# Performance work log

Hardware: AMD Instinct MI355X
Metric: run time of the kernel (lower is better)

The kernel has to match this reference:

```python
import jax, jax.numpy as jnp
import numpy as np

N = 524288
B, F, H, W = 2, 4, 64, 512
S = B * F * H * W  # dense voxel segment space
EPS = 1e-5


def _bn(x, g, b):
    # BatchNorm1d in training mode: normalize over the point dim with biased var
    m = x.mean(0)
    v = jnp.mean((x - m) ** 2, 0)
    return (x - m) / jnp.sqrt(v + EPS) * g + b


def setup_inputs() -> dict:
    key = jax.random.key(0)
    ks = jax.random.split(key, 20)
    pts = jax.random.normal(ks[0], (N, 4), dtype=jnp.float32) * 10.0
    bcol = jax.random.randint(ks[1], (N, 1), 0, B)
    fcol = jax.random.randint(ks[2], (N, 1), 0, F)
    hcol = jax.random.randint(ks[3], (N, 1), 0, H)
    wcol = jax.random.randint(ks[4], (N, 1), 0, W)
    coors = jnp.concatenate([bcol, fcol, hcol, wcol], -1).astype(jnp.int32)
    # original reads batch_size/frame_size from coors[-1]
    coors = coors.at[-1].set(jnp.array([B - 1, F - 1, H - 1, W - 1], dtype=jnp.int32))
    s = 0.02
    p = {
        'pre_gamma': jnp.ones((8,), jnp.float32),
        'pre_beta': jnp.zeros((8,), jnp.float32),
        'W1': jax.random.normal(ks[5], (8, 64), jnp.float32) * s,
        'g1': jnp.ones((64,), jnp.float32), 'b1': jnp.zeros((64,), jnp.float32),
        'W2': jax.random.normal(ks[6], (64, 128), jnp.float32) * s,
        'g2': jnp.ones((128,), jnp.float32), 'b2': jnp.zeros((128,), jnp.float32),
        'W3': jax.random.normal(ks[7], (128, 256), jnp.float32) * s,
        'g3': jnp.ones((256,), jnp.float32), 'b3': jnp.zeros((256,), jnp.float32),
        'W4': jax.random.normal(ks[8], (256, 256), jnp.float32) * s,
        'b4': jnp.zeros((256,), jnp.float32),
        'Wc': jax.random.normal(ks[9], (256, 64), jnp.float32) * s,
        'bc': jnp.zeros((64,), jnp.float32),
    }
    return {'pts': pts, 'pts_coors': coors, **p}


def reference(pts, pts_coors, pre_gamma, pre_beta, W1, g1, b1, W2, g2, b2,
              W3, g3, b3, W4, b4, Wc, bc):
    c = pts_coors
    lin = ((c[:, 0] * F + c[:, 1]) * H + c[:, 2]) * W + c[:, 3]  # (N,)
    counts = jax.ops.segment_sum(jnp.ones((pts.shape[0],), pts.dtype), lin, num_segments=S)
    # with_distance
    dist = jnp.linalg.norm(pts[:, :3], axis=1, keepdims=True)
    # with_cluster_center: scatter_mean then gather
    vsum = jax.ops.segment_sum(pts, lin, num_segments=S)
    vmean = vsum / jnp.clip(counts, 1.0)[:, None]
    f_cluster = pts[:, :3] - vmean[lin][:, :3]
    feats = jnp.concatenate([pts, dist, f_cluster], -1)  # (N, 8)
    feats = _bn(feats, pre_gamma, pre_beta)  # pre_norm
    x = jax.nn.relu(_bn(feats @ W1, g1, b1))
    x = jax.nn.relu(_bn(x @ W2, g2, b2))
    x = jax.nn.relu(_bn(x @ W3, g3, b3))
    point_feats = x @ W4 + b4  # (N, 256)
    # scatter_max over voxels
    seg = jax.ops.segment_max(point_feats, lin, num_segments=S)
    mask = (counts > 0)[:, None]
    voxel_feats = jnp.where(mask, seg, 0.0)
    comp = jax.nn.relu(voxel_feats @ Wc + bc)
    comp = jnp.where(mask, comp, 0.0)  # empty voxels stay zero in stack_frame
    stack = comp.reshape(B, F, H, W, -1)  # (B, F, H, W, Cc)
    residual = jnp.concatenate([stack[:, -1] - stack[:, f] for f in range(F - 1)], -1)
    residual_img = jnp.transpose(residual, (0, 3, 1, 2))  # (B, C, H, W)
    return residual_img
```

## Files before the change

kernel.cpp:

```cpp
#include <hip/hip_runtime.h>
#include <hip/hip_bf16.h>
#include <stdint.h>

typedef unsigned int u32;
typedef unsigned short u16;
typedef __attribute__((ext_vector_type(8))) short bf16x8;
typedef __attribute__((ext_vector_type(4))) float f32x4;

#define NPTS 524288
#define FF 4
#define HH 64
#define WW 512
#define SS 262144
#define EPSV 1e-5f
#define NB 8192
#define RCAP 80
#define VCAP 80

__device__ __forceinline__ float bf2f(u16 h){ return __uint_as_float(((u32)h)<<16); }
__device__ __forceinline__ u16 f2bf(float f){
  u32 u = __float_as_uint(f);
  return (u16)((u + 0x7FFFu + ((u>>16)&1u)) >> 16);
}

__device__ __forceinline__ void point_feats(int p, const float* __restrict__ pts,
    const u32* __restrict__ lin, const u32* __restrict__ counts,
    const float* __restrict__ vsum, float f[8], u32* vout){
  float4 pt = ((const float4*)pts)[p];
  u32 v = lin[p];
  float cnt = fmaxf((float)counts[v], 1.0f);
  float inv = 1.0f/cnt;
  float mx = vsum[v*3+0]*inv, my = vsum[v*3+1]*inv, mz = vsum[v*3+2]*inv;
  float dist = sqrtf(pt.x*pt.x + pt.y*pt.y + pt.z*pt.z);
  f[0]=pt.x; f[1]=pt.y; f[2]=pt.z; f[3]=pt.w; f[4]=dist;
  f[5]=pt.x-mx; f[6]=pt.y-my; f[7]=pt.z-mz;
  *vout = v;
}

__global__ __launch_bounds__(256) void k_lin(const float* __restrict__ pts,
                                             const int* __restrict__ coors,
                                             u32* __restrict__ lin,
                                             u32* __restrict__ counts,
                                             float* __restrict__ vsum){
  int p = blockIdx.x*256 + threadIdx.x;
  int4 c = ((const int4*)coors)[p];
  u32 v = ((u32)((c.x*FF + c.y)*HH + c.z))*WW + (u32)c.w;
  lin[p] = v;
  atomicAdd(&counts[v], 1u);
  float4 pt = ((const float4*)pts)[p];
  atomicAdd(&vsum[v*3+0], pt.x);
  atomicAdd(&vsum[v*3+1], pt.y);
  atomicAdd(&vsum[v*3+2], pt.z);
}

__global__ __launch_bounds__(256) void k_scan_a(const u32* __restrict__ counts,
                                                u32* __restrict__ blockSums){
  __shared__ u32 lds[256];
  int b = blockIdx.x, t = threadIdx.x;
  uint4 c4 = ((const uint4*)counts)[b*256 + t];
  lds[t] = c4.x + c4.y + c4.z + c4.w;
  __syncthreads();
  for(int s=128; s>0; s>>=1){ if(t<s) lds[t] += lds[t+s]; __syncthreads(); }
  if(t==0) blockSums[b] = lds[0];
}

__global__ void k_scan_b(u32* blockSums){
  if(threadIdx.x==0){
    u32 run = 0;
    for(int i=0;i<256;i++){ u32 v = blockSums[i]; blockSums[i] = run; run += v; }
  }
}

__global__ __launch_bounds__(256) void k_scan_c(const u32* __restrict__ counts,
                                                const u32* __restrict__ blockSums,
                                                u32* __restrict__ offsets,
                                                u32* __restrict__ cursor){
  __shared__ u32 lds[256];
  int b = blockIdx.x, t = threadIdx.x;
  uint4 c4 = ((const uint4*)counts)[b*256 + t];
  u32 mysum = c4.x + c4.y + c4.z + c4.w;
  lds[t] = mysum;
  __syncthreads();
  for(int d=1; d<256; d<<=1){
    u32 v = (t>=d) ? lds[t-d] : 0u;
    __syncthreads();
    lds[t] += v;
    __syncthreads();
  }
  u32 off = blockSums[b] + (t>0 ? lds[t-1] : 0u);
  u32 base = (u32)(b*1024 + t*4);
  offsets[base+0]=off; cursor[base+0]=off; off += c4.x;
  offsets[base+1]=off; cursor[base+1]=off; off += c4.y;
  offsets[base+2]=off; cursor[base+2]=off; off += c4.z;
  offsets[base+3]=off; cursor[base+3]=off; off += c4.w;
  if(base+4 == SS) offsets[SS] = off;
}

__global__ __launch_bounds__(256) void k_scatter(const u32* __restrict__ lin,
                                                 u32* __restrict__ cursor,
                                                 u32* __restrict__ order){
  int p = blockIdx.x*256 + threadIdx.x;
  u32 v = lin[p];
  u32 pos = atomicAdd(&cursor[v], 1u);
  order[pos] = p;
}

__global__ __launch_bounds__(256) void k_prep(const float* __restrict__ W2,
    const float* __restrict__ W3, const float* __restrict__ W4,
    const float* __restrict__ Wc,
    u16* __restrict__ W2t, u16* __restrict__ W3t, u16* __restrict__ W4t,
    u16* __restrict__ Wct){
  int i = blockIdx.x*256 + threadIdx.x;
  if(i < 8192){
    int k = i >> 7, n = i & 127;
    W2t[n*64 + k] = f2bf(W2[i]);
  } else if(i < 8192+32768){
    int j = i - 8192;
    int k = j >> 8, n = j & 255;
    W3t[n*128 + k] = f2bf(W3[j]);
  } else if(i < 8192+32768+65536){
    int j = i - (8192+32768);
    int k = j >> 8, n = j & 255;
    W4t[n*256 + k] = f2bf(W4[j]);
  } else if(i < 8192+32768+65536+16384){
    int j = i - (8192+32768+65536);
    int k = j >> 6, n = j & 63;
    Wct[n*256 + k] = f2bf(Wc[j]);
  }
}

__global__ __launch_bounds__(256) void k_stats0(const float* __restrict__ pts,
    const u32* __restrict__ lin, const u32* __restrict__ counts,
    const float* __restrict__ vsum, float* __restrict__ sum0, float* __restrict__ sq0){
  int p = blockIdx.x*256 + threadIdx.x;
  float f[8]; u32 v;
  point_feats(p, pts, lin, counts, vsum, f, &v);
  __shared__ float lsum[4][8], lsq[4][8];
  int lane = threadIdx.x & 63, wv = threadIdx.x >> 6;
  #pragma unroll
  for(int c=0;c<8;c++){
    float s = f[c], q = f[c]*f[c];
    #pragma unroll
    for(int d=32; d; d>>=1){ s += __shfl_xor(s,d); q += __shfl_xor(q,d); }
    if(lane==0){ lsum[wv][c]=s; lsq[wv][c]=q; }
  }
  __syncthreads();
  if(threadIdx.x<8){
    float s=0.f,q=0.f;
    for(int g=0;g<4;g++){ s+=lsum[g][threadIdx.x]; q+=lsq[g][threadIdx.x]; }
    atomicAdd(&sum0[threadIdx.x], s);
    atomicAdd(&sq0[threadIdx.x], q);
  }
}

__global__ void k_fold(const float* __restrict__ sum, const float* __restrict__ sq,
                       const float* __restrict__ g, const float* __restrict__ b,
                       float* __restrict__ a, float* __restrict__ c, int C){
  int i = blockIdx.x*64 + threadIdx.x;
  if(i < C){
    float m = sum[i]*(1.0f/NPTS);
    float v = sq[i]*(1.0f/NPTS) - m*m;
    v = fmaxf(v, 0.0f);
    float ai = g[i] / sqrtf(v + EPSV);
    a[i] = ai;
    c[i] = b[i] - m*ai;
  }
}

__global__ __launch_bounds__(256) void k_stats1(const float* __restrict__ pts,
    const u32* __restrict__ lin, const u32* __restrict__ counts,
    const float* __restrict__ vsum,
    const float* __restrict__ a0, const float* __restrict__ c0,
    const float* __restrict__ W1, float* __restrict__ sum1, float* __restrict__ sq1){
  __shared__ float ws[4][64], wq[4][64];
  int t = threadIdx.x;
  int p = blockIdx.x*256 + t;
  float f[8]; u32 v;
  point_feats(p, pts, lin, counts, vsum, f, &v);
  float y0[8];
  #pragma unroll
  for(int k=0;k<8;k++) y0[k] = a0[k]*f[k] + c0[k];
  float z[64];
  #pragma unroll
  for(int j=0;j<64;j++){
    float s=0.f;
    #pragma unroll
    for(int k=0;k<8;k++) s += y0[k]*W1[k*64+j];
    z[j]=s;
  }
  int lane = t&63, wv = t>>6;
  float ks=0.f, kq=0.f;
  #pragma unroll
  for(int c=0;c<64;c++){
    float s=z[c], q=z[c]*z[c];
    #pragma unroll
    for(int d=1; d<64; d<<=1){ s+=__shfl_xor(s,d); q+=__shfl_xor(q,d); }
    if(lane==c){ ks=s; kq=q; }
  }
  ws[wv][lane]=ks; wq[wv][lane]=kq;
  __syncthreads();
  if(t<64){
    float S=ws[0][t]+ws[1][t]+ws[2][t]+ws[3][t];
    float Q=wq[0][t]+wq[1][t]+wq[2][t]+wq[3][t];
    atomicAdd(&sum1[t],S); atomicAdd(&sq1[t],Q);
  }
}

__global__ __launch_bounds__(256,2) void k_mstats2(
    const float* __restrict__ pts, const u32* __restrict__ lin,
    const u32* __restrict__ counts, const float* __restrict__ vsum,
    const float* __restrict__ a0, const float* __restrict__ c0,
    const float* __restrict__ a1, const float* __restrict__ c1,
    const float* __restrict__ W1, const u16* __restrict__ W2t,
    float* __restrict__ sum2, float* __restrict__ sq2){
  __shared__ u16 T1[256*72];
  int tid = threadIdx.x, lane = tid&63, wid = tid>>6, l15 = lane&15, lg = lane>>4;
  float s2[2] = {0.f,0.f}, q2[2] = {0.f,0.f};

  for(int cch=0; cch<4; cch++){
    int p = blockIdx.x*1024 + cch*256 + tid;
    float f[8]; u32 v;
    point_feats(p, pts, lin, counts, vsum, f, &v);
    float y0[8];
    #pragma unroll
    for(int k=0;k<8;k++) y0[k] = a0[k]*f[k] + c0[k];
    u32 pk[32];
    #pragma unroll
    for(int jj=0;jj<32;jj++){
      float s0=0.f, s1=0.f;
      #pragma unroll
      for(int k=0;k<8;k++){ s0 += y0[k]*W1[k*64+2*jj]; s1 += y0[k]*W1[k*64+2*jj+1]; }
      float v0f = fmaxf(a1[2*jj]*s0   + c1[2*jj],   0.f);
      float v1f = fmaxf(a1[2*jj+1]*s1 + c1[2*jj+1], 0.f);
      pk[jj] = (u32)f2bf(v0f) | ((u32)f2bf(v1f)<<16);
    }
    __syncthreads();
    {
      uint4* dst = (uint4*)&T1[tid*72];
      #pragma unroll
      for(int q=0;q<8;q++) dst[q] = make_uint4(pk[4*q],pk[4*q+1],pk[4*q+2],pk[4*q+3]);
    }
    __syncthreads();
    #pragma unroll
    for(int ci=0; ci<2; ci++){
      int ch = (wid + 4*ci)*16 + l15;
      const u16* wb = W2t + (size_t)ch*64 + lg*8;
      bf16x8 b0 = *(const bf16x8*)(wb);
      bf16x8 b1 = *(const bf16x8*)(wb + 32);
      for(int rt=0; rt<16; rt++){
        const u16* ap = T1 + (rt*16 + l15)*72 + lg*8;
        bf16x8 af0 = *(const bf16x8*)(ap);
        bf16x8 af1 = *(const bf16x8*)(ap + 32);
        f32x4 acc = {0.f,0.f,0.f,0.f};
        acc = __builtin_amdgcn_mfma_f32_16x16x32_bf16(af0, b0, acc, 0,0,0);
        acc = __builtin_amdgcn_mfma_f32_16x16x32_bf16(af1, b1, acc, 0,0,0);
        #pragma unroll
        for(int i=0;i<4;i++){ s2[ci] += acc[i]; q2[ci] += acc[i]*acc[i]; }
      }
    }
  }
  #pragma unroll
  for(int ci=0; ci<2; ci++){
    float s = s2[ci], q = q2[ci];
    s += __shfl_xor(s,16); s += __shfl_xor(s,32);
    q += __shfl_xor(q,16); q += __shfl_xor(q,32);
    if(lg == 0){
      int ch = (wid + 4*ci)*16 + l15;
      atomicAdd(&sum2[ch], s);
      atomicAdd(&sq2[ch], q);
    }
  }
}

__global__ __launch_bounds__(256,1) void k_chain2(
    const float* __restrict__ pts, const u32* __restrict__ lin,
    const u32* __restrict__ counts, const float* __restrict__ vsum,
    const u32* __restrict__ order,
    const float* __restrict__ a0, const float* __restrict__ c0,
    const float* __restrict__ a1, const float* __restrict__ c1,
    const float* __restrict__ a2, const float* __restrict__ c2,
    const float* __restrict__ W1, const u16* __restrict__ W2t,
    const u16* __restrict__ W3t,
    u32* __restrict__ y2s,
    float* __restrict__ sum3, float* __restrict__ sq3){
  __shared__ u16 T1[256*72];
  __shared__ u16 T2[256*136];
  int tid = threadIdx.x, lane = tid&63, wid = tid>>6, l15 = lane&15, lg = lane>>4;
  float s3[4] = {0.f,0.f,0.f,0.f}, q3[4] = {0.f,0.f,0.f,0.f};

  for(int cch=0; cch<4; cch++){
    int rr = blockIdx.x*1024 + cch*256 + tid;
    int p = (int)order[rr];
    float f[8]; u32 v;
    point_feats(p, pts, lin, counts, vsum, f, &v);
    float y0[8];
    #pragma unroll
    for(int k=0;k<8;k++) y0[k] = a0[k]*f[k] + c0[k];
    u32 pk[32];
    #pragma unroll
    for(int jj=0;jj<32;jj++){
      float s0=0.f, s1=0.f;
      #pragma unroll
      for(int k=0;k<8;k++){ s0 += y0[k]*W1[k*64+2*jj]; s1 += y0[k]*W1[k*64+2*jj+1]; }
      float v0f = fmaxf(a1[2*jj]*s0   + c1[2*jj],   0.f);
      float v1f = fmaxf(a1[2*jj+1]*s1 + c1[2*jj+1], 0.f);
      pk[jj] = (u32)f2bf(v0f) | ((u32)f2bf(v1f)<<16);
    }
    __syncthreads();
    {
      uint4* dst = (uint4*)&T1[tid*72];
      #pragma unroll
      for(int q=0;q<8;q++) dst[q] = make_uint4(pk[4*q],pk[4*q+1],pk[4*q+2],pk[4*q+3]);
    }
    __syncthreads();
    #pragma unroll
    for(int ci=0; ci<2; ci++){
      int ch = (wid + 4*ci)*16 + l15;
      const u16* wb = W2t + (size_t)ch*64 + lg*8;
      bf16x8 b0 = *(const bf16x8*)(wb);
      bf16x8 b1 = *(const bf16x8*)(wb + 32);
      float a2v = a2[ch], c2v = c2[ch];
      for(int rt=0; rt<16; rt++){
        const u16* ap = T1 + (rt*16 + l15)*72 + lg*8;
        bf16x8 af0 = *(const bf16x8*)(ap);
        bf16x8 af1 = *(const bf16x8*)(ap + 32);
        f32x4 acc = {0.f,0.f,0.f,0.f};
        acc = __builtin_amdgcn_mfma_f32_16x16x32_bf16(af0, b0, acc, 0,0,0);
        acc = __builtin_amdgcn_mfma_f32_16x16x32_bf16(af1, b1, acc, 0,0,0);
        int rbase = rt*16 + lg*4;
        #pragma unroll
        for(int i=0;i<4;i++)
          T2[(rbase+i)*136 + ch] = f2bf(fmaxf(a2v*acc[i] + c2v, 0.f));
      }
    }
    __syncthreads();
    {
      const u32* T2w = (const u32*)T2;
      u32 base = (u32)blockIdx.x*1024u + (u32)cch*256u;
      for(int i=tid; i<256*64; i+=256){
        int row = i>>6, w = i&63;
        y2s[(size_t)(base+row)*64 + w] = T2w[row*68 + w];
      }
    }
    #pragma unroll
    for(int ci=0; ci<4; ci++){
      int ch = (wid + 4*ci)*16 + l15;
      const u16* wb = W3t + (size_t)ch*128 + lg*8;
      bf16x8 b[4];
      #pragma unroll
      for(int ks=0; ks<4; ks++) b[ks] = *(const bf16x8*)(wb + ks*32);
      for(int rt=0; rt<16; rt++){
        const u16* ap = T2 + (rt*16 + l15)*136 + lg*8;
        f32x4 acc = {0.f,0.f,0.f,0.f};
        #pragma unroll
        for(int ks=0; ks<4; ks++){
          bf16x8 af = *(const bf16x8*)(ap + ks*32);
          acc = __builtin_amdgcn_mfma_f32_16x16x32_bf16(af, b[ks], acc, 0,0,0);
        }
        #pragma unroll
        for(int i=0;i<4;i++){ s3[ci] += acc[i]; q3[ci] += acc[i]*acc[i]; }
      }
    }
  }
  #pragma unroll
  for(int ci=0; ci<4; ci++){
    float s = s3[ci], q = q3[ci];
    s += __shfl_xor(s,16); s += __shfl_xor(s,32);
    q += __shfl_xor(q,16); q += __shfl_xor(q,32);
    if(lg == 0){
      int ch = (wid + 4*ci)*16 + l15;
      atomicAdd(&sum3[ch], s);
      atomicAdd(&sq3[ch], q);
    }
  }
}

__global__ __launch_bounds__(512,4) void k_mega6(
    const u32* __restrict__ offsets, const u32* __restrict__ y2s,
    const float* __restrict__ a3, const float* __restrict__ c3,
    const u16* __restrict__ W3t, const u16* __restrict__ W4t,
    const u16* __restrict__ Wct,
    const float* __restrict__ b4, const float* __restrict__ bc,
    u16* __restrict__ comp){
  __shared__ __align__(16) char SM[78208];
  u16* T3  = (u16*)(SM);
  u16* T2s = (u16*)(SM + 42240);
  u16* Tz0 = (u16*)(SM + 42240);
  u16* Tz1 = (u16*)(SM + 53760);
  u16* TA  = (u16*)(SM + 65280);
  u32* vst = (u32*)(SM + 76800);
  float* bb = (float*)(SM + 77152);
  u32* hdr = (u32*)(SM + 78176);

  int tid = threadIdx.x, lane = tid & 63, wid = tid >> 6;
  int l15 = lane & 15, lg = lane >> 4;
  int cg = wid & 3, rh = wid >> 2;
  int nvt = rh ? 2 : 3, vt0 = rh ? 3 : 0;

  if(tid == 0){
    u32 t0 = (u32)blockIdx.x * 64u;
    u32 lo=0, hi=SS;
    while(lo<hi){ u32 mid=(lo+hi)>>1; if(offsets[mid] < t0) lo=mid+1; else hi=mid; }
    u32 vlo = lo, vhi;
    if(blockIdx.x == NB-1) vhi = SS;
    else {
      u32 t1 = t0 + 64u;
      lo = vlo; hi = SS;
      while(lo<hi){ u32 mid=(lo+hi)>>1; if(offsets[mid] < t1) lo=mid+1; else hi=mid; }
      vhi = lo;
    }
    hdr[0]=vlo; hdr[1]=vhi; hdr[2]=offsets[vlo]; hdr[3]=offsets[vhi];
  }
  if(tid < 256) bb[tid] = b4[tid];
  __syncthreads();
  u32 vlo=hdr[0], vhi=hdr[1], start=hdr[2], end=hdr[3];
  int R = (int)(end - start); if(R > RCAP) R = RCAP;
  int V = (int)(vhi - vlo);   if(V > VCAP) V = VCAP;

  if(tid <= VCAP){
    u32 o = (tid <= V) ? offsets[vlo + tid] : end;
    int s = (int)(o - start); if(s > RCAP) s = RCAP;
    vst[tid] = (u32)s;
  }

  {
    u32* T2w = (u32*)T2s;
    for(int i=tid; i<RCAP*64; i+=512){
      int row = i>>6, w = i&63;
      u32 val = (row < R) ? y2s[(size_t)(start+row)*64 + w] : 0u;
      T2w[row*68 + w] = val;
    }
  }
  __syncthreads();

  for(int ci=0; ci<2; ci++){
    int ch = (wid + 8*ci)*16 + l15;
    const u16* wb = W3t + (size_t)ch*128 + lg*8;
    bf16x8 b[4];
    #pragma unroll
    for(int ks=0; ks<4; ks++) b[ks] = *(const bf16x8*)(wb + ks*32);
    float a3v = a3[ch], c3v = c3[ch];
    for(int rt=0; rt<5; rt++){
      const u16* ap = T2s + (rt*16 + l15)*136 + lg*8;
      f32x4 acc = {0.f,0.f,0.f,0.f};
      #pragma unroll
      for(int ks=0; ks<4; ks++){
        bf16x8 af = *(const bf16x8*)(ap + ks*32);
        acc = __builtin_amdgcn_mfma_f32_16x16x32_bf16(af, b[ks], acc, 0,0,0);
      }
      int rbase = rt*16 + lg*4;
      #pragma unroll
      for(int i=0;i<4;i++)
        T3[(rbase+i)*264 + ch] = f2bf(fmaxf(a3v*acc[i] + c3v, 0.f));
    }
  }
  __syncthreads();

  f32x4 acc3[3];
  #pragma unroll
  for(int i=0;i<3;i++) acc3[i] = (f32x4){0.f,0.f,0.f,0.f};
  int ch4 = cg*16 + l15;

  for(int pr=0; pr<2; pr++){
    int oc0 = 2*pr, oc1 = 2*pr + 1;
    {
      const u16* wb0 = W4t + (size_t)(oc0*64 + ch4)*256 + lg*8;
      const u16* wb1 = W4t + (size_t)(oc1*64 + ch4)*256 + lg*8;
      bf16x8 b0[8], b1[8];
      #pragma unroll
      for(int ks=0; ks<8; ks++){
        b0[ks] = *(const bf16x8*)(wb0 + ks*32);
        b1[ks] = *(const bf16x8*)(wb1 + ks*32);
      }
      int rtB = rh ? 3 : 0, rtE = rh ? 5 : 3;
      for(int rt=rtB; rt<rtE; rt++){
        const u16* ap = T3 + (rt*16 + l15)*264 + lg*8;
        f32x4 aA = {0.f,0.f,0.f,0.f}, aB = {0.f,0.f,0.f,0.f};
        #pragma unroll
        for(int ks=0; ks<8; ks++){
          bf16x8 af = *(const bf16x8*)(ap + ks*32);
          aA = __builtin_amdgcn_mfma_f32_16x16x32_bf16(af, b0[ks], aA, 0,0,0);
          aB = __builtin_amdgcn_mfma_f32_16x16x32_bf16(af, b1[ks], aB, 0,0,0);
        }
        int rbase = rt*16 + lg*4;
        #pragma unroll
        for(int i=0;i<4;i++){
          Tz0[(rbase+i)*72 + ch4] = f2bf(aA[i]);
          Tz1[(rbase+i)*72 + ch4] = f2bf(aB[i]);
        }
      }
    }
    __syncthreads();
    for(int i=tid; i<VCAP*64; i+=512){
      int v = i>>6, k = i&63;
      u32 r0 = vst[v], r1 = vst[v+1];
      u16 outv = 0;
      if(r1 > r0){
        float m = -3.0e38f;
        for(u32 r=r0; r<r1; r++) m = fmaxf(m, bf2f(Tz0[r*72+k]));
        outv = f2bf(m + bb[oc0*64+k]);
      }
      TA[v*72+k] = outv;
    }
    __syncthreads();
    {
      const u16* wb = Wct + (size_t)ch4*256 + oc0*64 + lg*8;
      bf16x8 c0f = *(const bf16x8*)(wb);
      bf16x8 c1f = *(const bf16x8*)(wb + 32);
      #pragma unroll
      for(int s=0; s<3; s++){
        if(s < nvt){
          int vt = vt0 + s;
          const u16* ap = TA + (vt*16 + l15)*72 + lg*8;
          bf16x8 af0 = *(const bf16x8*)(ap);
          bf16x8 af1 = *(const bf16x8*)(ap + 32);
          acc3[s] = __builtin_amdgcn_mfma_f32_16x16x32_bf16(af0, c0f, acc3[s], 0,0,0);
          acc3[s] = __builtin_amdgcn_mfma_f32_16x16x32_bf16(af1, c1f, acc3[s], 0,0,0);
        }
      }
    }
    __syncthreads();
    for(int i=tid; i<VCAP*64; i+=512){
      int v = i>>6, k = i&63;
      u32 r0 = vst[v], r1 = vst[v+1];
      u16 outv = 0;
      if(r1 > r0){
        float m = -3.0e38f;
        for(u32 r=r0; r<r1; r++) m = fmaxf(m, bf2f(Tz1[r*72+k]));
        outv = f2bf(m + bb[oc1*64+k]);
      }
      TA[v*72+k] = outv;
    }
    __syncthreads();
    {
      const u16* wb = Wct + (size_t)ch4*256 + oc1*64 + lg*8;
      bf16x8 c0f = *(const bf16x8*)(wb);
      bf16x8 c1f = *(const bf16x8*)(wb + 32);
      #pragma unroll
      for(int s=0; s<3; s++){
        if(s < nvt){
          int vt = vt0 + s;
          const u16* ap = TA + (vt*16 + l15)*72 + lg*8;
          bf16x8 af0 = *(const bf16x8*)(ap);
          bf16x8 af1 = *(const bf16x8*)(ap + 32);
          acc3[s] = __builtin_amdgcn_mfma_f32_16x16x32_bf16(af0, c0f, acc3[s], 0,0,0);
          acc3[s] = __builtin_amdgcn_mfma_f32_16x16x32_bf16(af1, c1f, acc3[s], 0,0,0);
        }
      }
    }
    __syncthreads();
  }

  {
    float bcv = bc[ch4];
    #pragma unroll
    for(int s=0; s<3; s++){
      if(s < nvt){
        int vt = vt0 + s;
        int vbase = vt*16 + lg*4;
        #pragma unroll
        for(int i=0;i<4;i++){
          int vox = vbase + i;
          if(vox < V){
            bool nz = vst[vox+1] > vst[vox];
            float val = nz ? fmaxf(acc3[s][i] + bcv, 0.f) : 0.f;
            comp[(size_t)(vlo+vox)*64 + ch4] = f2bf(val);
          }
        }
      }
    }
  }
}

__global__ __launch_bounds__(256) void k_resid(const u16* __restrict__ comp,
                                               float* __restrict__ out){
  __shared__ u32 cl[4*128*32];
  int t = threadIdx.x;
  int blk = blockIdx.x;
  int wq = blk & 3, h = (blk>>2) & 63, b = blk>>8;
  int w0 = wq*128;
  for(int fr=0; fr<4; fr++){
    const u32* src = (const u32*)comp + ((size_t)(((b*4+fr)*64 + h)*512 + w0))*32;
    for(int i=t; i<4096; i+=256){
      int vox = i>>5, wd = i&31;
      cl[fr*4096 + vox*32 + (wd ^ (vox&31))] = src[i];
    }
  }
  __syncthreads();
  int wl = t & 127, half = t >> 7;
  int mv = wl & 31;
  for(int ch = half; ch < 64; ch += 2){
    u32 wr3 = cl[3*4096 + wl*32 + ((ch>>1) ^ mv)];
    float r3 = bf2f((ch&1) ? (u16)(wr3>>16) : (u16)(wr3&0xFFFFu));
    #pragma unroll
    for(int fr=0; fr<3; fr++){
      u32 wrf = cl[fr*4096 + wl*32 + ((ch>>1) ^ mv)];
      float vf = bf2f((ch&1) ? (u16)(wrf>>16) : (u16)(wrf&0xFFFFu));
      out[(((size_t)(b*192 + fr*64 + ch))*64 + h)*512 + w0 + wl] = r3 - vf;
    }
  }
}

extern "C" void kernel_launch(void* const* d_in, const int* in_sizes, int n_in,
                              void* d_out, int out_size, void* d_ws, size_t ws_size,
                              hipStream_t stream){
  const float* pts  = (const float*)d_in[0];
  const int*  coors = (const int*)d_in[1];
  const float* g0 = (const float*)d_in[2];
  const float* b0 = (const float*)d_in[3];
  const float* W1 = (const float*)d_in[4];
  const float* g1 = (const float*)d_in[5];
  const float* b1 = (const float*)d_in[6];
  const float* W2 = (const float*)d_in[7];
  const float* g2 = (const float*)d_in[8];
  const float* b2 = (const float*)d_in[9];
  const float* W3 = (const float*)d_in[10];
  const float* g3 = (const float*)d_in[11];
  const float* b3 = (const float*)d_in[12];
  const float* W4 = (const float*)d_in[13];
  const float* b4 = (const float*)d_in[14];
  const float* Wc = (const float*)d_in[15];
  const float* bc = (const float*)d_in[16];
  float* out = (float*)d_out;
  (void)in_sizes; (void)n_in; (void)out_size; (void)ws_size;

  char* ws = (char*)d_ws;
  size_t off = 0;
  auto alloc = [&](size_t bytes)->void*{
    void* p = ws + off;
    off += (bytes + 255) & ~(size_t)255;
    return p;
  };
  u32*  counts  = (u32*)alloc((size_t)SS*4);
  float* vsum   = (float*)alloc((size_t)SS*3*4);
  float* stats  = (float*)alloc(8192);
  size_t zero_bytes = off;
  u32*  lin     = (u32*)alloc((size_t)NPTS*4);
  u32*  offsets = (u32*)alloc((size_t)(SS+1)*4);
  u32*  cursor  = (u32*)alloc((size_t)SS*4);
  u32*  order   = (u32*)alloc((size_t)NPTS*4);
  u32*  blockSums = (u32*)alloc(1024);
  u16*  comp    = (u16*)alloc((size_t)SS*64*2);
  u16*  W2t = (u16*)alloc(8192*2);
  u16*  W3t = (u16*)alloc(32768*2);
  u16*  W4t = (u16*)alloc(65536*2);
  u16*  Wct = (u16*)alloc(16384*2);
  u32*  y2s = (u32*)alloc((size_t)NPTS*64*4);

  float* sum0=stats+0,   *sq0=stats+8,    *a0=stats+16,   *c0=stats+24;
  float* sum1=stats+32,  *sq1=stats+96,   *a1=stats+160,  *c1=stats+224;
  float* sum2=stats+288, *sq2=stats+416,  *a2=stats+544,  *c2=stats+672;
  float* sum3=stats+800, *sq3=stats+1056, *a3=stats+1312, *c3=stats+1568;

  hipMemsetAsync(d_ws, 0, zero_bytes, stream);

  k_prep   <<<480, 256,0,stream>>>(W2, W3, W4, Wc, W2t, W3t, W4t, Wct);
  k_lin    <<<2048,256,0,stream>>>(pts, coors, lin, counts, vsum);
  k_scan_a <<<256, 256,0,stream>>>(counts, blockSums);
  k_scan_b <<<1,   64, 0,stream>>>(blockSums);
  k_scan_c <<<256, 256,0,stream>>>(counts, blockSums, offsets, cursor);
  k_scatter<<<2048,256,0,stream>>>(lin, cursor, order);

  k_stats0 <<<2048,256,0,stream>>>(pts, lin, counts, vsum, sum0, sq0);
  k_fold   <<<1,   64, 0,stream>>>(sum0, sq0, g0, b0, a0, c0, 8);
  k_stats1 <<<2048,256,0,stream>>>(pts, lin, counts, vsum, a0, c0, W1, sum1, sq1);
  k_fold   <<<1,   64, 0,stream>>>(sum1, sq1, g1, b1, a1, c1, 64);
  k_mstats2<<<512, 256,0,stream>>>(pts, lin, counts, vsum, a0,c0,a1,c1, W1, W2t, sum2, sq2);
  k_fold   <<<2,   64, 0,stream>>>(sum2, sq2, g2, b2, a2, c2, 128);
  k_chain2 <<<512, 256,0,stream>>>(pts, lin, counts, vsum, order,
                                   a0,c0,a1,c1,a2,c2, W1, W2t, W3t,
                                   y2s, sum3, sq3);
  k_fold   <<<4,   64, 0,stream>>>(sum3, sq3, g3, b3, a3, c3, 256);

  k_mega6  <<<NB,  512,0,stream>>>(offsets, y2s, a3,c3, W3t, W4t, Wct, b4, bc, comp);
  k_resid  <<<512, 256,0,stream>>>(comp, out);
}
```

Measured before the change: 1.092 ms.

## Cache per-point features and widen chain kernel to 512 threads

k_stats0 now writes the 8 per-point pre-norm features to a global buffer, and later stages read them back instead of recomputing from pts, lin, counts and vsum with scattered gathers. k_stats1 is rewritten so each lane owns one W1 output channel and loops over points, which removes the 64-step cross-lane shuffle reduction per channel. k_chain2 is launched with 512 threads so each wave handles fewer layer-2 and layer-3 output tiles. The cost is an extra 16 MB feature buffer written and read several times, and half the threads in k_chain2 sit idle during the layer-1 phase.

```diff
diff --git a/kernel.cpp b/kernel.cpp
--- a/kernel.cpp
+++ b/kernel.cpp
@@ -131,10 +131,14 @@
 
 __global__ __launch_bounds__(256) void k_stats0(const float* __restrict__ pts,
     const u32* __restrict__ lin, const u32* __restrict__ counts,
-    const float* __restrict__ vsum, float* __restrict__ sum0, float* __restrict__ sq0){
+    const float* __restrict__ vsum, float* __restrict__ feats,
+    float* __restrict__ sum0, float* __restrict__ sq0){
   int p = blockIdx.x*256 + threadIdx.x;
   float f[8]; u32 v;
   point_feats(p, pts, lin, counts, vsum, f, &v);
+  float4* fo = (float4*)&feats[(size_t)p*8];
+  fo[0] = make_float4(f[0],f[1],f[2],f[3]);
+  fo[1] = make_float4(f[4],f[5],f[6],f[7]);
   __shared__ float lsum[4][8], lsq[4][8];
   int lane = threadIdx.x & 63, wv = threadIdx.x >> 6;
   #pragma unroll
@@ -167,48 +171,36 @@
   }
 }
 
-__global__ __launch_bounds__(256) void k_stats1(const float* __restrict__ pts,
-    const u32* __restrict__ lin, const u32* __restrict__ counts,
-    const float* __restrict__ vsum,
+__global__ __launch_bounds__(256) void k_stats1b(const float* __restrict__ feats,
     const float* __restrict__ a0, const float* __restrict__ c0,
-    const float* __restrict__ W1, float* __restrict__ sum1, float* __restrict__ sq1){
-  __shared__ float ws[4][64], wq[4][64];
-  int t = threadIdx.x;
-  int p = blockIdx.x*256 + t;
-  float f[8]; u32 v;
-  point_feats(p, pts, lin, counts, vsum, f, &v);
-  float y0[8];
+    const float* __restrict__ W1,
+    float* __restrict__ sum1, float* __restrict__ sq1){
+  __shared__ float ls[4][64], lq[4][64];
+  int tid = threadIdx.x, lane = tid & 63, wv = tid >> 6;
+  float w1c[8], a0r[8], c0r[8];
   #pragma unroll
-  for(int k=0;k<8;k++) y0[k] = a0[k]*f[k] + c0[k];
-  float z[64];
-  #pragma unroll
-  for(int j=0;j<64;j++){
-    float s=0.f;
-    #pragma unroll
-    for(int k=0;k<8;k++) s += y0[k]*W1[k*64+j];
-    z[j]=s;
-  }
-  int lane = t&63, wv = t>>6;
-  float ks=0.f, kq=0.f;
-  #pragma unroll
-  for(int c=0;c<64;c++){
-    float s=z[c], q=z[c]*z[c];
-    #pragma unroll
-    for(int d=1; d<64; d<<=1){ s+=__shfl_xor(s,d); q+=__shfl_xor(q,d); }
-    if(lane==c){ ks=s; kq=q; }
-  }
-  ws[wv][lane]=ks; wq[wv][lane]=kq;
-  __syncthreads();
-  if(t<64){
-    float S=ws[0][t]+ws[1][t]+ws[2][t]+ws[3][t];
-    float Q=wq[0][t]+wq[1][t]+wq[2][t]+wq[3][t];
-    atomicAdd(&sum1[t],S); atomicAdd(&sq1[t],Q);
+  for(int k=0;k<8;k++){ w1c[k]=W1[k*64+lane]; a0r[k]=a0[k]; c0r[k]=c0[k]; }
+  float s = 0.f, q = 0.f;
+  size_t p0 = (size_t)blockIdx.x*1024 + (size_t)wv*256;
+  for(int pp=0; pp<256; pp++){
+    const float* fr = &feats[(p0+pp)*8];
+    float z = 0.f;
+    #pragma unroll
+    for(int k=0;k<8;k++) z += (a0r[k]*fr[k] + c0r[k]) * w1c[k];
+    s += z; q += z*z;
+  }
+  ls[wv][lane]=s; lq[wv][lane]=q;
+  __syncthreads();
+  if(tid < 64){
+    float S = ls[0][tid]+ls[1][tid]+ls[2][tid]+ls[3][tid];
+    float Q = lq[0][tid]+lq[1][tid]+lq[2][tid]+lq[3][tid];
+    atomicAdd(&sum1[tid], S);
+    atomicAdd(&sq1[tid], Q);
   }
 }
 
 __global__ __launch_bounds__(256,2) void k_mstats2(
-    const float* __restrict__ pts, const u32* __restrict__ lin,
-    const u32* __restrict__ counts, const float* __restrict__ vsum,
+    const float* __restrict__ feats,
     const float* __restrict__ a0, const float* __restrict__ c0,
     const float* __restrict__ a1, const float* __restrict__ c1,
     const float* __restrict__ W1, const u16* __restrict__ W2t,
@@ -219,8 +211,9 @@
 
   for(int cch=0; cch<4; cch++){
     int p = blockIdx.x*1024 + cch*256 + tid;
-    float f[8]; u32 v;
-    point_feats(p, pts, lin, counts, vsum, f, &v);
+    const float4* fr = (const float4*)&feats[(size_t)p*8];
+    float4 fa = fr[0], fb = fr[1];
+    float f[8] = {fa.x,fa.y,fa.z,fa.w,fb.x,fb.y,fb.z,fb.w};
     float y0[8];
     #pragma unroll
     for(int k=0;k<8;k++) y0[k] = a0[k]*f[k] + c0[k];
@@ -272,10 +265,8 @@
   }
 }
 
-__global__ __launch_bounds__(256,1) void k_chain2(
-    const float* __restrict__ pts, const u32* __restrict__ lin,
-    const u32* __restrict__ counts, const float* __restrict__ vsum,
-    const u32* __restrict__ order,
+__global__ __launch_bounds__(512,1) void k_chain2(
+    const float* __restrict__ feats, const u32* __restrict__ order,
     const float* __restrict__ a0, const float* __restrict__ c0,
     const float* __restrict__ a1, const float* __restrict__ c1,
     const float* __restrict__ a2, const float* __restrict__ c2,
@@ -286,36 +277,38 @@
   __shared__ u16 T1[256*72];
   __shared__ u16 T2[256*136];
   int tid = threadIdx.x, lane = tid&63, wid = tid>>6, l15 = lane&15, lg = lane>>4;
-  float s3[4] = {0.f,0.f,0.f,0.f}, q3[4] = {0.f,0.f,0.f,0.f};
+  float s3[2] = {0.f,0.f}, q3[2] = {0.f,0.f};
 
   for(int cch=0; cch<4; cch++){
-    int rr = blockIdx.x*1024 + cch*256 + tid;
-    int p = (int)order[rr];
-    float f[8]; u32 v;
-    point_feats(p, pts, lin, counts, vsum, f, &v);
-    float y0[8];
-    #pragma unroll
-    for(int k=0;k<8;k++) y0[k] = a0[k]*f[k] + c0[k];
     u32 pk[32];
-    #pragma unroll
-    for(int jj=0;jj<32;jj++){
-      float s0=0.f, s1=0.f;
-      #pragma unroll
-      for(int k=0;k<8;k++){ s0 += y0[k]*W1[k*64+2*jj]; s1 += y0[k]*W1[k*64+2*jj+1]; }
-      float v0f = fmaxf(a1[2*jj]*s0   + c1[2*jj],   0.f);
-      float v1f = fmaxf(a1[2*jj+1]*s1 + c1[2*jj+1], 0.f);
-      pk[jj] = (u32)f2bf(v0f) | ((u32)f2bf(v1f)<<16);
+    if(tid < 256){
+      int rr = blockIdx.x*1024 + cch*256 + tid;
+      int p = (int)order[rr];
+      const float4* fr = (const float4*)&feats[(size_t)p*8];
+      float4 fa = fr[0], fb = fr[1];
+      float f[8] = {fa.x,fa.y,fa.z,fa.w,fb.x,fb.y,fb.z,fb.w};
+      float y0[8];
+      #pragma unroll
+      for(int k=0;k<8;k++) y0[k] = a0[k]*f[k] + c0[k];
+      #pragma unroll
+      for(int jj=0;jj<32;jj++){
+        float s0=0.f, s1=0.f;
+        #pragma unroll
+        for(int k=0;k<8;k++){ s0 += y0[k]*W1[k*64+2*jj]; s1 += y0[k]*W1[k*64+2*jj+1]; }
+        float v0f = fmaxf(a1[2*jj]*s0   + c1[2*jj],   0.f);
+        float v1f = fmaxf(a1[2*jj+1]*s1 + c1[2*jj+1], 0.f);
+        pk[jj] = (u32)f2bf(v0f) | ((u32)f2bf(v1f)<<16);
+      }
+    }
+    __syncthreads();
+    if(tid < 256){
+      uint4* dst = (uint4*)&T1[tid*72];
+      #pragma unroll
+      for(int q=0;q<8;q++) dst[q] = make_uint4(pk[4*q],pk[4*q+1],pk[4*q+2],pk[4*q+3]);
     }
     __syncthreads();
     {
-      uint4* dst = (uint4*)&T1[tid*72];
-      #pragma unroll
-      for(int q=0;q<8;q++) dst[q] = make_uint4(pk[4*q],pk[4*q+1],pk[4*q+2],pk[4*q+3]);
-    }
-    __syncthreads();
-    #pragma unroll
-    for(int ci=0; ci<2; ci++){
-      int ch = (wid + 4*ci)*16 + l15;
+      int ch = wid*16 + l15;
       const u16* wb = W2t + (size_t)ch*64 + lg*8;
       bf16x8 b0 = *(const bf16x8*)(wb);
       bf16x8 b1 = *(const bf16x8*)(wb + 32);
@@ -337,14 +330,14 @@
     {
       const u32* T2w = (const u32*)T2;
       u32 base = (u32)blockIdx.x*1024u + (u32)cch*256u;
-      for(int i=tid; i<256*64; i+=256){
+      for(int i=tid; i<256*64; i+=512){
         int row = i>>6, w = i&63;
         y2s[(size_t)(base+row)*64 + w] = T2w[row*68 + w];
       }
     }
     #pragma unroll
-    for(int ci=0; ci<4; ci++){
-      int ch = (wid + 4*ci)*16 + l15;
+    for(int ci=0; ci<2; ci++){
+      int ch = (wid + 8*ci)*16 + l15;
       const u16* wb = W3t + (size_t)ch*128 + lg*8;
       bf16x8 b[4];
       #pragma unroll
@@ -363,12 +356,12 @@
     }
   }
   #pragma unroll
-  for(int ci=0; ci<4; ci++){
+  for(int ci=0; ci<2; ci++){
     float s = s3[ci], q = q3[ci];
     s += __shfl_xor(s,16); s += __shfl_xor(s,32);
     q += __shfl_xor(q,16); q += __shfl_xor(q,32);
     if(lg == 0){
-      int ch = (wid + 4*ci)*16 + l15;
+      int ch = (wid + 8*ci)*16 + l15;
       atomicAdd(&sum3[ch], s);
       atomicAdd(&sq3[ch], q);
     }
@@ -645,6 +638,7 @@
   u16*  W3t = (u16*)alloc(32768*2);
   u16*  W4t = (u16*)alloc(65536*2);
   u16*  Wct = (u16*)alloc(16384*2);
+  float* feats = (float*)alloc((size_t)NPTS*8*4);
   u32*  y2s = (u32*)alloc((size_t)NPTS*64*4);
 
   float* sum0=stats+0,   *sq0=stats+8,    *a0=stats+16,   *c0=stats+24;
@@ -661,14 +655,13 @@
   k_scan_c <<<256, 256,0,stream>>>(counts, blockSums, offsets, cursor);
   k_scatter<<<2048,256,0,stream>>>(lin, cursor, order);
 
-  k_stats0 <<<2048,256,0,stream>>>(pts, lin, counts, vsum, sum0, sq0);
+  k_stats0 <<<2048,256,0,stream>>>(pts, lin, counts, vsum, feats, sum0, sq0);
   k_fold   <<<1,   64, 0,stream>>>(sum0, sq0, g0, b0, a0, c0, 8);
-  k_stats1 <<<2048,256,0,stream>>>(pts, lin, counts, vsum, a0, c0, W1, sum1, sq1);
+  k_stats1b<<<512, 256,0,stream>>>(feats, a0, c0, W1, sum1, sq1);
   k_fold   <<<1,   64, 0,stream>>>(sum1, sq1, g1, b1, a1, c1, 64);
-  k_mstats2<<<512, 256,0,stream>>>(pts, lin, counts, vsum, a0,c0,a1,c1, W1, W2t, sum2, sq2);
+  k_mstats2<<<512, 256,0,stream>>>(feats, a0,c0,a1,c1, W1, W2t, sum2, sq2);
   k_fold   <<<2,   64, 0,stream>>>(sum2, sq2, g2, b2, a2, c2, 128);
-  k_chain2 <<<512, 256,0,stream>>>(pts, lin, counts, vsum, order,
-                                   a0,c0,a1,c1,a2,c2, W1, W2t, W3t,
+  k_chain2 <<<512, 512,0,stream>>>(feats, order, a0,c0,a1,c1,a2,c2, W1, W2t, W3t,
                                    y2s, sum3, sq3);
   k_fold   <<<4,   64, 0,stream>>>(sum3, sq3, g3, b3, a3, c3, 256);
 
```

New measurement: 1.066 ms. 1.02x faster.
